# Performance work log

Measured on AMD Instinct MI355X. Metric: run time of the kernel, lower is better.

Reference implementation:

```python
import jax, jax.numpy as jnp
import numpy as np

UNITS = 50

def setup_inputs() -> dict:
    key = jax.random.key(0)
    ks = jax.random.split(key, 6)
    B, T, F = 4096, 128, 64
    scale = 0.1
    return {
        "x": jax.random.normal(ks[0], (B, T, F), dtype=jnp.float32),
        "W": jax.random.normal(ks[1], (F, 3 * UNITS), dtype=jnp.float32) * scale,
        "U": jax.random.normal(ks[2], (UNITS, 3 * UNITS), dtype=jnp.float32) * scale,
        "b": jax.random.normal(ks[3], (2, 3 * UNITS), dtype=jnp.float32) * scale,
        "Wd": jax.random.normal(ks[4], (UNITS, 1), dtype=jnp.float32) * scale,
        "bd": jnp.zeros((1,), dtype=jnp.float32),
    }

def reference(x, W, U, b, Wd, bd):
    # Keras GRU, reset_after=True, activation=relu, recurrent_activation=sigmoid.
    B, T, F = x.shape
    u = UNITS
    # Precompute input projections for all timesteps: [B,T,3u]
    xp = jnp.einsum('btf,fk->btk', x, W) + b[0]
    xp = jnp.moveaxis(xp, 1, 0)  # [T,B,3u]
    bi = b[1]

    def step(h, xt):
        hp = h @ U + bi                     # [B,3u]
        xz, xr, xh = xt[:, :u], xt[:, u:2*u], xt[:, 2*u:]
        hz, hr, hh = hp[:, :u], hp[:, u:2*u], hp[:, 2*u:]
        z = jax.nn.sigmoid(xz + hz)
        r = jax.nn.sigmoid(xr + hr)
        hcand = jax.nn.relu(xh + r * hh)
        h_new = z * h + (1.0 - z) * hcand
        return h_new, None

    h0 = jnp.zeros((B, u), dtype=x.dtype)
    hT, _ = jax.lax.scan(step, h0, xp)
    # Dropout is identity at inference; Dense head:
    return hT @ Wd + bd
```

## Files before the change

### kernel.cpp

```cpp
#include <hip/hip_runtime.h>
#include <math.h>

typedef _Float16 v8h __attribute__((ext_vector_type(8)));
typedef float v4f __attribute__((ext_vector_type(4)));

#define UNITS    50
#define K3       150
#define FDIM     64
#define TSTEPS   128
#define BATCH    4096
#define NB       16
#define H16S     72
#define H32S     52

#if __has_builtin(__builtin_amdgcn_exp2f)
__device__ __forceinline__ float fast_exp2(float x) { return __builtin_amdgcn_exp2f(x); }
#else
__device__ __forceinline__ float fast_exp2(float x) { return exp2f(x); }
#endif
#if __has_builtin(__builtin_amdgcn_rcpf)
__device__ __forceinline__ float fast_rcp(float x) { return __builtin_amdgcn_rcpf(x); }
#else
__device__ __forceinline__ float fast_rcp(float x) { return 1.0f / x; }
#endif

__device__ __forceinline__ void sync_lds() {
    asm volatile("s_waitcnt lgkmcnt(0)" ::: "memory");
    __builtin_amdgcn_s_barrier();
}

__global__ __launch_bounds__(256, 1)
void gru_nodrain(const float* __restrict__ x, const float* __restrict__ W,
                 const float* __restrict__ U, const float* __restrict__ bv,
                 const float* __restrict__ Wd, const float* __restrict__ bd,
                 float* __restrict__ out) {
    __shared__ _Float16 hs16[2][NB * H16S];
    __shared__ float    hs32[NB * H32S];

    const int tid  = threadIdx.x;
    const int nt   = tid >> 6;
    const int lane = tid & 63;
    const int n    = lane & 15;
    const int quad = lane >> 4;
    const int b0   = blockIdx.x * NB;
    const int c    = nt * 16 + n;

    for (int i = tid; i < NB * H16S; i += 256) {
        _Float16 v = ((i % H16S) == 50) ? (_Float16)1.f : (_Float16)0.f;
        hs16[0][i] = v;
        hs16[1][i] = v;
    }

    v8h Bz[4], Br[4], Bh[4];
    #pragma unroll
    for (int kt = 0; kt < 4; ++kt) {
        v8h fz, fr, fh;
        #pragma unroll
        for (int j = 0; j < 8; ++j) {
            const int k = kt * 32 + quad * 8 + j;
            float vz = 0.f, vr = 0.f, vh = 0.f;
            if (c < UNITS) {
                if (k < FDIM) {
                    vz = W[k * K3 + c];
                    vr = W[k * K3 + 50 + c];
                    vh = W[k * K3 + 100 + c];
                } else if (k < FDIM + UNITS) {
                    const int ur = k - FDIM;
                    vz = U[ur * K3 + c];
                    vr = U[ur * K3 + 50 + c];
                    vh = U[ur * K3 + 100 + c];
                } else if (k == FDIM + UNITS) {
                    vh = bv[250 + c];
                }
            }
            fz[j] = (_Float16)vz; fr[j] = (_Float16)vr; fh[j] = (_Float16)vh;
        }
        Bz[kt] = fz; Br[kt] = fr; Bh[kt] = fh;
    }

    const float CE = -1.44269504f;
    float bzc = 0.f, brc = 0.f, bx = 0.f;
    if (c < UNITS) {
        bzc = CE * (bv[c]      + bv[150 + c]);
        brc = CE * (bv[50 + c] + bv[200 + c]);
        bx  = bv[100 + c];
    }

    v4f h32 = {0.f, 0.f, 0.f, 0.f};

    const float* xbase = x + ((size_t)(b0 + n) * TSTEPS) * FDIM + quad * 8;
    v4f px[2][4];
    #pragma unroll
    for (int s = 0; s < 2; ++s) {
        const float* xp = xbase + (size_t)s * FDIM;
        px[s][0] = *(const v4f*)(xp + 0);
        px[s][1] = *(const v4f*)(xp + 4);
        px[s][2] = *(const v4f*)(xp + 32);
        px[s][3] = *(const v4f*)(xp + 36);
    }

    __syncthreads();

    #pragma unroll 2
    for (int t = 0; t < TSTEPS; ++t) {
        const int pb = t & 1;
        const _Float16* hrd = hs16[t & 1];
        _Float16*       hwr = hs16[(t + 1) & 1];

        v8h A2 = *(const v8h*)(&hrd[n * H16S + quad * 8]);
        v8h A3 = *(const v8h*)(&hrd[n * H16S + 32 + quad * 8]);
        v8h A0, A1;
        #pragma unroll
        for (int j = 0; j < 4; ++j) {
            A0[j]     = (_Float16)px[pb][0][j];
            A0[j + 4] = (_Float16)px[pb][1][j];
            A1[j]     = (_Float16)px[pb][2][j];
            A1[j + 4] = (_Float16)px[pb][3][j];
        }

        if (t + 2 < TSTEPS) {
            const float* xp = xbase + (size_t)(t + 2) * FDIM;
            px[pb][0] = *(const v4f*)(xp + 0);
            px[pb][1] = *(const v4f*)(xp + 4);
            px[pb][2] = *(const v4f*)(xp + 32);
            px[pb][3] = *(const v4f*)(xp + 36);
        }

        const v4f zero4 = {0.f, 0.f, 0.f, 0.f};
        v4f axx = {bx, bx, bx, bx};
        v4f azx = __builtin_amdgcn_mfma_f32_16x16x32_f16(A0, Bz[0], zero4, 0, 0, 0);
        azx     = __builtin_amdgcn_mfma_f32_16x16x32_f16(A1, Bz[1], azx,   0, 0, 0);
        v4f arx = __builtin_amdgcn_mfma_f32_16x16x32_f16(A0, Br[0], zero4, 0, 0, 0);
        arx     = __builtin_amdgcn_mfma_f32_16x16x32_f16(A1, Br[1], arx,   0, 0, 0);
        axx     = __builtin_amdgcn_mfma_f32_16x16x32_f16(A0, Bh[0], axx,   0, 0, 0);
        axx     = __builtin_amdgcn_mfma_f32_16x16x32_f16(A1, Bh[1], axx,   0, 0, 0);
        v4f azh = __builtin_amdgcn_mfma_f32_16x16x32_f16(A2, Bz[2], zero4, 0, 0, 0);
        azh     = __builtin_amdgcn_mfma_f32_16x16x32_f16(A3, Bz[3], azh,   0, 0, 0);
        v4f arh = __builtin_amdgcn_mfma_f32_16x16x32_f16(A2, Br[2], zero4, 0, 0, 0);
        arh     = __builtin_amdgcn_mfma_f32_16x16x32_f16(A3, Br[3], arh,   0, 0, 0);
        v4f ahh = __builtin_amdgcn_mfma_f32_16x16x32_f16(A2, Bh[2], zero4, 0, 0, 0);
        ahh     = __builtin_amdgcn_mfma_f32_16x16x32_f16(A3, Bh[3], ahh,   0, 0, 0);

        #pragma unroll
        for (int r = 0; r < 4; ++r) {
            const float az = azx[r] + azh[r];
            const float ar = arx[r] + arh[r];
            const float ez = fast_exp2(fmaf(az, CE, bzc));
            const float er = fast_exp2(fmaf(ar, CE, brc));
            const float pz = 1.f + ez;
            const float pr = 1.f + er;
            const float d  = fast_rcp(pz * pr);
            const float zg = d * pr;
            const float rg = d * pz;
            const float hc = fmaxf(fmaf(rg, ahh[r], axx[r]), 0.f);
            const float hn = fmaf(zg, h32[r] - hc, hc);
            h32[r] = hn;
            if (c < UNITS)
                hwr[(quad * 4 + r) * H16S + c] = (_Float16)hn;
        }
        sync_lds();
    }

    if (c < UNITS) {
        #pragma unroll
        for (int r = 0; r < 4; ++r)
            hs32[(quad * 4 + r) * H32S + c] = h32[r];
    }
    __syncthreads();
    if (tid < NB) {
        float acc = bd[0];
        #pragma unroll
        for (int u = 0; u < UNITS; ++u)
            acc = fmaf(hs32[tid * H32S + u], Wd[u], acc);
        out[b0 + tid] = acc;
    }
}

extern "C" void kernel_launch(void* const* d_in, const int* in_sizes, int n_in,
                              void* d_out, int out_size, void* d_ws, size_t ws_size,
                              hipStream_t stream) {
    const float* x    = (const float*)d_in[0];
    const float* W    = (const float*)d_in[1];
    const float* U    = (const float*)d_in[2];
    const float* bv   = (const float*)d_in[3];
    const float* Wd   = (const float*)d_in[4];
    const float* bd   = (const float*)d_in[5];
    float* out = (float*)d_out;

    dim3 grid(BATCH / NB);
    dim3 block(256);
    gru_nodrain<<<grid, block, 0, stream>>>(x, W, U, bv, Wd, bd, out);
}
```

Measured before the change: 277.7 us.

## Precompute input projections four steps ahead in a register ring

The x·W projection for each timestep is now computed four steps ahead and held in a 4-deep register ring. The per-step critical path then contains only the recurrent h·U MFMAs, which are split into independent halves so the two chained MFMAs no longer wait on each other. The x prefetch is extended to six steps ahead, and the loop is unrolled by four so the ring index stays static. This takes the input-projection MFMAs off the serial recurrence dependency chain, at the cost of higher register pressure.

After: 277.7 us. No clear change (-0.0%).

```diff
diff --git a/kernel.cpp b/kernel.cpp
--- a/kernel.cpp
+++ b/kernel.cpp
@@ -30,10 +30,10 @@
 }
 
 __global__ __launch_bounds__(256, 1)
-void gru_nodrain(const float* __restrict__ x, const float* __restrict__ W,
-                 const float* __restrict__ U, const float* __restrict__ bv,
-                 const float* __restrict__ Wd, const float* __restrict__ bd,
-                 float* __restrict__ out) {
+void gru_ring(const float* __restrict__ x, const float* __restrict__ W,
+              const float* __restrict__ U, const float* __restrict__ bv,
+              const float* __restrict__ Wd, const float* __restrict__ bd,
+              float* __restrict__ out) {
     __shared__ _Float16 hs16[2][NB * H16S];
     __shared__ float    hs32[NB * H32S];
 
@@ -89,10 +89,38 @@
     v4f h32 = {0.f, 0.f, 0.f, 0.f};
 
     const float* xbase = x + ((size_t)(b0 + n) * TSTEPS) * FDIM + quad * 8;
+    const v4f z4 = {0.f, 0.f, 0.f, 0.f};
+    const v4f ch = {bx, bx, bx, bx};
+
+    v4f xz[4], xr[4], xh[4];
+    #pragma unroll
+    for (int s = 0; s < 4; ++s) {
+        const float* xp = xbase + (size_t)s * FDIM;
+        v4f p0 = *(const v4f*)(xp + 0);
+        v4f p1 = *(const v4f*)(xp + 4);
+        v4f p2 = *(const v4f*)(xp + 32);
+        v4f p3 = *(const v4f*)(xp + 36);
+        v8h A0, A1;
+        #pragma unroll
+        for (int j = 0; j < 4; ++j) {
+            A0[j]     = (_Float16)p0[j];
+            A0[j + 4] = (_Float16)p1[j];
+            A1[j]     = (_Float16)p2[j];
+            A1[j + 4] = (_Float16)p3[j];
+        }
+        v4f tz = __builtin_amdgcn_mfma_f32_16x16x32_f16(A0, Bz[0], z4, 0, 0, 0);
+        tz     = __builtin_amdgcn_mfma_f32_16x16x32_f16(A1, Bz[1], tz, 0, 0, 0);
+        v4f tr = __builtin_amdgcn_mfma_f32_16x16x32_f16(A0, Br[0], z4, 0, 0, 0);
+        tr     = __builtin_amdgcn_mfma_f32_16x16x32_f16(A1, Br[1], tr, 0, 0, 0);
+        v4f th = __builtin_amdgcn_mfma_f32_16x16x32_f16(A0, Bh[0], ch, 0, 0, 0);
+        th     = __builtin_amdgcn_mfma_f32_16x16x32_f16(A1, Bh[1], th, 0, 0, 0);
+        xz[s] = tz; xr[s] = tr; xh[s] = th;
+    }
+
     v4f px[2][4];
     #pragma unroll
     for (int s = 0; s < 2; ++s) {
-        const float* xp = xbase + (size_t)s * FDIM;
+        const float* xp = xbase + (size_t)(4 + s) * FDIM;
         px[s][0] = *(const v4f*)(xp + 0);
         px[s][1] = *(const v4f*)(xp + 4);
         px[s][2] = *(const v4f*)(xp + 32);
@@ -101,50 +129,58 @@
 
     __syncthreads();
 
-    #pragma unroll 2
+    #pragma unroll 4
     for (int t = 0; t < TSTEPS; ++t) {
-        const int pb = t & 1;
+        const int s  = t & 3;
+        const int pp = t & 1;
         const _Float16* hrd = hs16[t & 1];
         _Float16*       hwr = hs16[(t + 1) & 1];
 
         v8h A2 = *(const v8h*)(&hrd[n * H16S + quad * 8]);
         v8h A3 = *(const v8h*)(&hrd[n * H16S + 32 + quad * 8]);
-        v8h A0, A1;
-        #pragma unroll
-        for (int j = 0; j < 4; ++j) {
-            A0[j]     = (_Float16)px[pb][0][j];
-            A0[j + 4] = (_Float16)px[pb][1][j];
-            A1[j]     = (_Float16)px[pb][2][j];
-            A1[j + 4] = (_Float16)px[pb][3][j];
-        }
-
-        if (t + 2 < TSTEPS) {
-            const float* xp = xbase + (size_t)(t + 2) * FDIM;
-            px[pb][0] = *(const v4f*)(xp + 0);
-            px[pb][1] = *(const v4f*)(xp + 4);
-            px[pb][2] = *(const v4f*)(xp + 32);
-            px[pb][3] = *(const v4f*)(xp + 36);
-        }
-
-        const v4f zero4 = {0.f, 0.f, 0.f, 0.f};
-        v4f axx = {bx, bx, bx, bx};
-        v4f azx = __builtin_amdgcn_mfma_f32_16x16x32_f16(A0, Bz[0], zero4, 0, 0, 0);
-        azx     = __builtin_amdgcn_mfma_f32_16x16x32_f16(A1, Bz[1], azx,   0, 0, 0);
-        v4f arx = __builtin_amdgcn_mfma_f32_16x16x32_f16(A0, Br[0], zero4, 0, 0, 0);
-        arx     = __builtin_amdgcn_mfma_f32_16x16x32_f16(A1, Br[1], arx,   0, 0, 0);
-        axx     = __builtin_amdgcn_mfma_f32_16x16x32_f16(A0, Bh[0], axx,   0, 0, 0);
-        axx     = __builtin_amdgcn_mfma_f32_16x16x32_f16(A1, Bh[1], axx,   0, 0, 0);
-        v4f azh = __builtin_amdgcn_mfma_f32_16x16x32_f16(A2, Bz[2], zero4, 0, 0, 0);
-        azh     = __builtin_amdgcn_mfma_f32_16x16x32_f16(A3, Bz[3], azh,   0, 0, 0);
-        v4f arh = __builtin_amdgcn_mfma_f32_16x16x32_f16(A2, Br[2], zero4, 0, 0, 0);
-        arh     = __builtin_amdgcn_mfma_f32_16x16x32_f16(A3, Br[3], arh,   0, 0, 0);
-        v4f ahh = __builtin_amdgcn_mfma_f32_16x16x32_f16(A2, Bh[2], zero4, 0, 0, 0);
-        ahh     = __builtin_amdgcn_mfma_f32_16x16x32_f16(A3, Bh[3], ahh,   0, 0, 0);
+
+        const bool do_refill = (t + 4 < TSTEPS);
+        v8h N0, N1;
+        if (do_refill) {
+            #pragma unroll
+            for (int j = 0; j < 4; ++j) {
+                N0[j]     = (_Float16)px[pp][0][j];
+                N0[j + 4] = (_Float16)px[pp][1][j];
+                N1[j]     = (_Float16)px[pp][2][j];
+                N1[j + 4] = (_Float16)px[pp][3][j];
+            }
+        }
+        if (t + 6 < TSTEPS) {
+            const float* xp = xbase + (size_t)(t + 6) * FDIM;
+            px[pp][0] = *(const v4f*)(xp + 0);
+            px[pp][1] = *(const v4f*)(xp + 4);
+            px[pp][2] = *(const v4f*)(xp + 32);
+            px[pp][3] = *(const v4f*)(xp + 36);
+        }
+
+        v4f azA = __builtin_amdgcn_mfma_f32_16x16x32_f16(A2, Bz[2], xz[s], 0, 0, 0);
+        v4f azB = __builtin_amdgcn_mfma_f32_16x16x32_f16(A3, Bz[3], z4,    0, 0, 0);
+        v4f arA = __builtin_amdgcn_mfma_f32_16x16x32_f16(A2, Br[2], xr[s], 0, 0, 0);
+        v4f arB = __builtin_amdgcn_mfma_f32_16x16x32_f16(A3, Br[3], z4,    0, 0, 0);
+        v4f ahA = __builtin_amdgcn_mfma_f32_16x16x32_f16(A2, Bh[2], z4,    0, 0, 0);
+        v4f ahB = __builtin_amdgcn_mfma_f32_16x16x32_f16(A3, Bh[3], z4,    0, 0, 0);
+        const v4f hx = xh[s];
+
+        if (do_refill) {
+            v4f tz = __builtin_amdgcn_mfma_f32_16x16x32_f16(N0, Bz[0], z4, 0, 0, 0);
+            tz     = __builtin_amdgcn_mfma_f32_16x16x32_f16(N1, Bz[1], tz, 0, 0, 0);
+            v4f tr = __builtin_amdgcn_mfma_f32_16x16x32_f16(N0, Br[0], z4, 0, 0, 0);
+            tr     = __builtin_amdgcn_mfma_f32_16x16x32_f16(N1, Br[1], tr, 0, 0, 0);
+            v4f th = __builtin_amdgcn_mfma_f32_16x16x32_f16(N0, Bh[0], ch, 0, 0, 0);
+            th     = __builtin_amdgcn_mfma_f32_16x16x32_f16(N1, Bh[1], th, 0, 0, 0);
+            xz[s] = tz; xr[s] = tr; xh[s] = th;
+        }
 
         #pragma unroll
         for (int r = 0; r < 4; ++r) {
-            const float az = azx[r] + azh[r];
-            const float ar = arx[r] + arh[r];
+            const float az = azA[r] + azB[r];
+            const float ar = arA[r] + arB[r];
+            const float hh = ahA[r] + ahB[r];
             const float ez = fast_exp2(fmaf(az, CE, bzc));
             const float er = fast_exp2(fmaf(ar, CE, brc));
             const float pz = 1.f + ez;
@@ -152,7 +188,7 @@
             const float d  = fast_rcp(pz * pr);
             const float zg = d * pr;
             const float rg = d * pz;
-            const float hc = fmaxf(fmaf(rg, ahh[r], axx[r]), 0.f);
+            const float hc = fmaxf(fmaf(rg, hh, hx[r]), 0.f);
             const float hn = fmaf(zg, h32[r] - hc, hc);
             h32[r] = hn;
             if (c < UNITS)
@@ -189,5 +225,5 @@
 
     dim3 grid(BATCH / NB);
     dim3 block(256);
-    gru_nodrain<<<grid, block, 0, stream>>>(x, W, U, bv, Wd, bd, out);
+    gru_ring<<<grid, block, 0, stream>>>(x, W, U, bv, Wd, bd, out);
 }
```
